# Kernel optimization log

Measured on AMD Instinct MI355X. Metric: run time of the kernel, lower is better.

## Reference

```python
import jax, jax.numpy as jnp
import numpy as np

B, S, D, F, E, R = 16, 1024, 1024, 4096, 8, 32
LORA_ALPHA = 16
SCALING = LORA_ALPHA / R  # 0.5


def setup_inputs() -> dict:
    key = jax.random.key(0)
    ks = jax.random.split(key, 16)
    sd = 0.02
    return {
        "x": jax.random.normal(ks[0], (B, S, D), jnp.float32),
        "router_w": jax.random.normal(ks[1], (E, D), jnp.float32) * sd,
        "router_b": jnp.zeros((E,), jnp.float32),
        "fc1_w": jax.random.normal(ks[2], (F, D), jnp.float32) * sd,
        "fc1_b": jnp.zeros((F,), jnp.float32),
        "fc2_w": jax.random.normal(ks[3], (D, F), jnp.float32) * sd,
        "fc2_b": jnp.zeros((D,), jnp.float32),
        "down_A_w": jax.random.normal(ks[4], (E, R, D), jnp.float32) * sd,
        "down_A_b": jnp.zeros((E, R), jnp.float32),
        "down_B_w": jax.random.normal(ks[5], (E, F, R), jnp.float32) * sd,
        "down_B_b": jnp.zeros((E, F), jnp.float32),
        "up_A_w": jax.random.normal(ks[6], (E, R, F), jnp.float32) * sd,
        "up_A_b": jnp.zeros((E, R), jnp.float32),
        "up_B_w": jax.random.normal(ks[7], (E, D, R), jnp.float32) * sd,
        "up_B_b": jnp.zeros((E, D), jnp.float32),
    }


def _lora_moe_sparse(inp, onehot, A_w, A_b, B_w, B_b):
    # inp: [b,t,c_in]; onehot: [b,t,E] hard top-1 dispatch mask
    # h: per-expert rank activations [b,t,E,R] (small: R=32)
    h = jnp.einsum('btc,erc->bter', inp, A_w) + A_b
    g = h * onehot[..., None]  # zero out non-selected experts (sparse dispatch)
    out = jnp.einsum('bter,eor->bto', g, B_w)
    out = out + jnp.einsum('bte,eo->bto', onehot, B_b)
    return out * SCALING


def reference(x, router_w, router_b, fc1_w, fc1_b, fc2_w, fc2_b,
              down_A_w, down_A_b, down_B_w, down_B_b,
              up_A_w, up_A_b, up_B_w, up_B_b):
    # router + top-1 hard routing (straight-through expert_choice)
    logits = jnp.einsum('btd,ed->bte', x, router_w) + router_b
    routing = jax.nn.softmax(logits, axis=-1)
    idx = jnp.argmax(routing, axis=-1)                       # [b,t]
    y_hard = jax.nn.one_hot(idx, E, dtype=x.dtype)           # [b,t,E]
    expert_choice = y_hard - jax.lax.stop_gradient(routing) + routing

    # down proj: frozen fc1 + sparse LoRA combine (dropout p=0.05 -> eval/identity)
    h1 = jnp.einsum('btd,fd->btf', x, fc1_w) + fc1_b
    h1 = h1 + _lora_moe_sparse(x, y_hard, down_A_w, down_A_b, down_B_w, down_B_b)
    a = jax.nn.gelu(h1, approximate=False)

    # up proj: frozen fc2 + sparse LoRA combine
    out = jnp.einsum('btf,df->btd', a, fc2_w) + fc2_b
    out = out + _lora_moe_sparse(a, y_hard, up_A_w, up_A_b, up_B_w, up_B_b)
    return out, (routing, expert_choice)
```

## Files before the change

### kernel.cpp

```cpp
#include <hip/hip_runtime.h>
#include <hip/hip_bf16.h>
#include <math.h>


#define M_TOK 16384
#define DIM_D 1024
#define DIM_F 4096
#define NEXP 8
#define RANK 32
#define NER 256

typedef __attribute__((ext_vector_type(8))) short bf16x8;
typedef __attribute__((ext_vector_type(4))) float f32x4;

__device__ inline short f2bs(float x) {
  __hip_bfloat16 h = __float2bfloat16(x);
  return *reinterpret_cast<short*>(&h);
}

__device__ inline void async16(const void* g, void* l) {
  __builtin_amdgcn_global_load_lds(
      (__attribute__((address_space(1))) void*)(g),
      (__attribute__((address_space(3))) void*)(l), 16, 0, 0);
}

__global__ __launch_bounds__(256) void convert_bf16(
    const float* __restrict__ in, short* __restrict__ out, int n8)
{
  const int i = blockIdx.x * 256 + threadIdx.x;
  if (i >= n8) return;
  const float4* p = (const float4*)in + 2 * (size_t)i;
  float4 u = p[0], v = p[1];
  bf16x8 r;
  r[0] = f2bs(u.x); r[1] = f2bs(u.y); r[2] = f2bs(u.z); r[3] = f2bs(u.w);
  r[4] = f2bs(v.x); r[5] = f2bs(v.y); r[6] = f2bs(v.z); r[7] = f2bs(v.w);
  *(bf16x8*)(out + 8 * (size_t)i) = r;
}

__global__ __launch_bounds__(256) void router_kernel(
    const float* __restrict__ X,
    const float* __restrict__ RW,
    const float* __restrict__ RB,
    float* __restrict__ routing_out,
    float* __restrict__ ec_out,
    int* __restrict__ idx_out)
{
  const int wave = threadIdx.x >> 6;
  const int lane = threadIdx.x & 63;
  const int t = blockIdx.x * 4 + wave;

  const float4* xp = (const float4*)(X + (size_t)t * DIM_D);
  float4 xv[4];
#pragma unroll
  for (int i = 0; i < 4; ++i) xv[i] = xp[lane + 64 * i];

  float logit[NEXP];
#pragma unroll
  for (int e = 0; e < NEXP; ++e) {
    const float4* wp = (const float4*)(RW + (size_t)e * DIM_D);
    double p = 0.0;
#pragma unroll
    for (int i = 0; i < 4; ++i) {
      float4 w = wp[lane + 64 * i];
      p += (double)xv[i].x * w.x + (double)xv[i].y * w.y +
           (double)xv[i].z * w.z + (double)xv[i].w * w.w;
    }
#pragma unroll
    for (int off = 32; off > 0; off >>= 1) p += __shfl_xor(p, off);
    logit[e] = (float)p + RB[e];
  }
  float m = logit[0];
  int am = 0;
#pragma unroll
  for (int e = 1; e < NEXP; ++e)
    if (logit[e] > m) { m = logit[e]; am = e; }
  float pr[NEXP], s = 0.f;
#pragma unroll
  for (int e = 0; e < NEXP; ++e) { pr[e] = expf(logit[e] - m); s += pr[e]; }
  const float inv = 1.f / s;
  if (lane < NEXP) {
    float r = pr[lane] * inv;
    routing_out[(size_t)t * NEXP + lane] = r;
    float y = (lane == am) ? 1.f : 0.f;
    ec_out[(size_t)t * NEXP + lane] = (y - r) + r;
  }
  if (lane == 0) idx_out[t] = am;
}

template <int KMAIN, int DO_LORA, int EPI>
__global__ __launch_bounds__(256, 2) void gemm_bf16(
    const short* __restrict__ A, const short* __restrict__ Bm,
    const short* __restrict__ G2, const short* __restrict__ LW,
    const float* __restrict__ LB, const float* __restrict__ bias,
    const int* __restrict__ idx, void* __restrict__ outv, int N)
{
  __shared__ __align__(16) short As[128 * 32];
  __shared__ __align__(16) short Bs[128 * 32];

  const int tid = threadIdx.x;
  const int m0 = blockIdx.y * 128;
  const int n0 = blockIdx.x * 128;
  const int lane = tid & 63;
  const int wv = tid >> 6;
  const int quad = lane >> 4;
  const int lrow = lane & 15;
  const int wr = wv >> 1;
  const int wc = wv & 1;
  const int r0 = tid >> 2;
  const int c4 = (tid & 3) * 8;

  f32x4 acc[4][4];
#pragma unroll
  for (int i = 0; i < 4; ++i)
#pragma unroll
    for (int j = 0; j < 4; ++j) acc[i][j] = (f32x4){0.f, 0.f, 0.f, 0.f};

  constexpr int IT_MAIN = KMAIN / 32;
  constexpr int IT_TOT = IT_MAIN + (DO_LORA ? NEXP : 0);
  for (int it = 0; it < IT_TOT; ++it) {
    const short *a0, *a1, *b0, *b1;
    if (!DO_LORA || it < IT_MAIN) {
      const int k = it * 32;
      a0 = A + (size_t)(m0 + r0) * KMAIN + k + c4;
      a1 = a0 + (size_t)64 * KMAIN;
      b0 = Bm + (size_t)(n0 + r0) * KMAIN + k + c4;
      b1 = b0 + (size_t)64 * KMAIN;
    } else {
      const int e = it - IT_MAIN;
      a0 = G2 + (size_t)(m0 + r0) * NER + e * RANK + c4;
      a1 = a0 + 64 * NER;
      b0 = LW + ((size_t)e * N + n0 + r0) * RANK + c4;
      b1 = b0 + 64 * RANK;
    }
    async16(a0, &As[tid * 8]);
    async16(a1, &As[2048 + tid * 8]);
    async16(b0, &Bs[tid * 8]);
    async16(b1, &Bs[2048 + tid * 8]);
    __syncthreads();

    bf16x8 af[4], bfv[4];
#pragma unroll
    for (int i = 0; i < 4; ++i)
      af[i] = *(const bf16x8*)&As[(wr * 64 + i * 16 + lrow) * 32 + quad * 8];
#pragma unroll
    for (int j = 0; j < 4; ++j)
      bfv[j] = *(const bf16x8*)&Bs[(wc * 64 + j * 16 + lrow) * 32 + quad * 8];
#pragma unroll
    for (int i = 0; i < 4; ++i)
#pragma unroll
      for (int j = 0; j < 4; ++j)
        acc[i][j] = __builtin_amdgcn_mfma_f32_16x16x32_bf16(af[i], bfv[j],
                                                            acc[i][j], 0, 0, 0);
    __syncthreads();
  }

  float cb[4];
#pragma unroll
  for (int j = 0; j < 4; ++j) cb[j] = bias[n0 + wc * 64 + j * 16 + lrow];

#pragma unroll
  for (int i = 0; i < 4; ++i) {
#pragma unroll
    for (int reg = 0; reg < 4; ++reg) {
      const int t = m0 + wr * 64 + i * 16 + quad * 4 + reg;
      const int e = idx[t];
#pragma unroll
      for (int j = 0; j < 4; ++j) {
        const int gc = n0 + wc * 64 + j * 16 + lrow;
        float v = acc[i][j][reg];
        if (EPI == 2) {
          v = ((gc >> 5) == e) ? 0.5f * (v + cb[j]) : 0.f;
          ((short*)outv)[(size_t)t * N + gc] = f2bs(v);
        } else {
          v += cb[j] + 0.5f * LB[(size_t)e * N + gc];
          if (EPI == 1) {
            v = 0.5f * v * (1.0f + erff(v * 0.70710678118654752f));
            ((short*)outv)[(size_t)t * N + gc] = f2bs(v);
          } else {
            ((float*)outv)[(size_t)t * N + gc] = v;
          }
        }
      }
    }
  }
}

extern "C" void kernel_launch(void* const* d_in, const int* in_sizes, int n_in,
                              void* d_out, int out_size, void* d_ws, size_t ws_size,
                              hipStream_t stream) {
  (void)in_sizes; (void)n_in; (void)out_size; (void)ws_size;
  const float* x        = (const float*)d_in[0];
  const float* router_w = (const float*)d_in[1];
  const float* router_b = (const float*)d_in[2];
  const float* fc1_w    = (const float*)d_in[3];
  const float* fc1_b    = (const float*)d_in[4];
  const float* fc2_w    = (const float*)d_in[5];
  const float* fc2_b    = (const float*)d_in[6];
  const float* down_A_w = (const float*)d_in[7];
  const float* down_A_b = (const float*)d_in[8];
  const float* down_B_w = (const float*)d_in[9];
  const float* down_B_b = (const float*)d_in[10];
  const float* up_A_w   = (const float*)d_in[11];
  const float* up_A_b   = (const float*)d_in[12];
  const float* up_B_w   = (const float*)d_in[13];
  const float* up_B_b   = (const float*)d_in[14];

  char* ws = (char*)d_ws;
  size_t off = 0;
  int* idxp = (int*)ws;                    off += (size_t)M_TOK * 4;
  short* g2d  = (short*)(ws + off);        off += (size_t)M_TOK * NER * 2;
  short* g2u  = (short*)(ws + off);        off += (size_t)M_TOK * NER * 2;
  short* a_ws = (short*)(ws + off);        off += (size_t)M_TOK * DIM_F * 2;
  short* xb   = (short*)(ws + off);        off += (size_t)M_TOK * DIM_D * 2;
  short* fc1b = (short*)(ws + off);        off += (size_t)DIM_F * DIM_D * 2;
  short* fc2b = (short*)(ws + off);        off += (size_t)DIM_D * DIM_F * 2;
  short* dAb  = (short*)(ws + off);        off += (size_t)NER * DIM_D * 2;
  short* uAb  = (short*)(ws + off);        off += (size_t)NER * DIM_F * 2;
  short* dBb  = (short*)(ws + off);        off += (size_t)NEXP * DIM_F * RANK * 2;
  short* uBb  = (short*)(ws + off);        off += (size_t)NEXP * DIM_D * RANK * 2;

  float* out = (float*)d_out;
  float* routing = out + (size_t)M_TOK * DIM_D;
  float* ec = routing + (size_t)M_TOK * NEXP;

  auto conv = [&](const float* src, short* dst, size_t n) {
    int n8 = (int)(n / 8);
    convert_bf16<<<(n8 + 255) / 256, 256, 0, stream>>>(src, dst, n8);
  };
  conv(x, xb, (size_t)M_TOK * DIM_D);
  conv(fc1_w, fc1b, (size_t)DIM_F * DIM_D);
  conv(fc2_w, fc2b, (size_t)DIM_D * DIM_F);
  conv(down_A_w, dAb, (size_t)NER * DIM_D);
  conv(up_A_w, uAb, (size_t)NER * DIM_F);
  conv(down_B_w, dBb, (size_t)NEXP * DIM_F * RANK);
  conv(up_B_w, uBb, (size_t)NEXP * DIM_D * RANK);

  router_kernel<<<M_TOK / 4, 256, 0, stream>>>(x, router_w, router_b, routing,
                                               ec, idxp);
  gemm_bf16<DIM_D, 0, 2><<<dim3(NER / 128, M_TOK / 128), 256, 0, stream>>>(
      xb, dAb, nullptr, nullptr, nullptr, down_A_b, idxp, g2d, NER);
  gemm_bf16<DIM_D, 1, 1><<<dim3(DIM_F / 128, M_TOK / 128), 256, 0, stream>>>(
      xb, fc1b, g2d, dBb, down_B_b, fc1_b, idxp, a_ws, DIM_F);
  gemm_bf16<DIM_F, 0, 2><<<dim3(NER / 128, M_TOK / 128), 256, 0, stream>>>(
      a_ws, uAb, nullptr, nullptr, nullptr, up_A_b, idxp, g2u, NER);
  gemm_bf16<DIM_F, 1, 0><<<dim3(DIM_D / 128, M_TOK / 128), 256, 0, stream>>>(
      a_ws, fc2b, g2u, uBb, up_B_b, fc2_b, idxp, out, DIM_D);
}
```

Measured before the change: 763.7 us.

## Concatenate LoRA into K dimension and use 256x256 pipelined GEMM

The LoRA rank activations and LoRA-B weights are packed as extra K columns of the activation and weight matrices, so the main GEMMs run a single uniform K loop. The main GEMMs move to a 512-thread, 256x256-tile kernel with double-buffered LDS, swizzled addressing, interleaved async loads and MFMA priority hints, plus workgroup remapping for L2 locality. The x-to-bf16 conversion is folded into the router kernel, removing a separate pass. The larger tile raises register and LDS pressure, and the hand-written barrier and waitcnt schedule must be exactly right.

```diff
diff --git a/kernel.cpp b/kernel.cpp
--- a/kernel.cpp
+++ b/kernel.cpp
@@ -9,8 +9,11 @@
 #define NEXP 8
 #define RANK 32
 #define NER 256
+#define K1 1280
+#define K2 4352
 
 typedef __attribute__((ext_vector_type(8))) short bf16x8;
+typedef __attribute__((ext_vector_type(4))) short sh4;
 typedef __attribute__((ext_vector_type(4))) float f32x4;
 
 __device__ inline short f2bs(float x) {
@@ -24,17 +27,38 @@
       (__attribute__((address_space(3))) void*)(l), 16, 0, 0);
 }
 
-__global__ __launch_bounds__(256) void convert_bf16(
-    const float* __restrict__ in, short* __restrict__ out, int n8)
+__global__ __launch_bounds__(256) void convert_pitched(
+    const float* __restrict__ in, short* __restrict__ out,
+    int c8, int opitch, int n8)
 {
   const int i = blockIdx.x * 256 + threadIdx.x;
   if (i >= n8) return;
-  const float4* p = (const float4*)in + 2 * (size_t)i;
+  const int row = i / c8;
+  const int c = (i % c8) * 8;
+  const float4* p = (const float4*)(in + (size_t)row * (c8 * 8) + c);
   float4 u = p[0], v = p[1];
   bf16x8 r;
   r[0] = f2bs(u.x); r[1] = f2bs(u.y); r[2] = f2bs(u.z); r[3] = f2bs(u.w);
   r[4] = f2bs(v.x); r[5] = f2bs(v.y); r[6] = f2bs(v.z); r[7] = f2bs(v.w);
-  *(bf16x8*)(out + 8 * (size_t)i) = r;
+  *(bf16x8*)(out + (size_t)row * opitch + c) = r;
+}
+
+__global__ __launch_bounds__(256) void pack_lorab(
+    const float* __restrict__ in, short* __restrict__ out,
+    int Nn, int opitch, int ooff, int n8)
+{
+  const int i = blockIdx.x * 256 + threadIdx.x;
+  if (i >= n8) return;
+  const int e = i / (Nn * 4);
+  const int rem = i % (Nn * 4);
+  const int n = rem >> 2;
+  const int r8 = (rem & 3) * 8;
+  const float4* p = (const float4*)(in + ((size_t)e * Nn + n) * RANK + r8);
+  float4 u = p[0], v = p[1];
+  bf16x8 r;
+  r[0] = f2bs(u.x); r[1] = f2bs(u.y); r[2] = f2bs(u.z); r[3] = f2bs(u.w);
+  r[4] = f2bs(v.x); r[5] = f2bs(v.y); r[6] = f2bs(v.z); r[7] = f2bs(v.w);
+  *(bf16x8*)(out + (size_t)n * opitch + ooff + e * RANK + r8) = r;
 }
 
 __global__ __launch_bounds__(256) void router_kernel(
@@ -43,7 +67,8 @@
     const float* __restrict__ RB,
     float* __restrict__ routing_out,
     float* __restrict__ ec_out,
-    int* __restrict__ idx_out)
+    int* __restrict__ idx_out,
+    short* __restrict__ XB)
 {
   const int wave = threadIdx.x >> 6;
   const int lane = threadIdx.x & 63;
@@ -53,6 +78,14 @@
   float4 xv[4];
 #pragma unroll
   for (int i = 0; i < 4; ++i) xv[i] = xp[lane + 64 * i];
+
+#pragma unroll
+  for (int i = 0; i < 4; ++i) {
+    sh4 o;
+    o[0] = f2bs(xv[i].x); o[1] = f2bs(xv[i].y);
+    o[2] = f2bs(xv[i].z); o[3] = f2bs(xv[i].w);
+    *(sh4*)&XB[(size_t)t * K1 + (lane + 64 * i) * 4] = o;
+  }
 
   float logit[NEXP];
 #pragma unroll
@@ -87,12 +120,11 @@
   if (lane == 0) idx_out[t] = am;
 }
 
-template <int KMAIN, int DO_LORA, int EPI>
-__global__ __launch_bounds__(256, 2) void gemm_bf16(
+template <int KM, int LDA, int OPITCH, int OOFF>
+__global__ __launch_bounds__(256, 2) void lora_a_gemm(
     const short* __restrict__ A, const short* __restrict__ Bm,
-    const short* __restrict__ G2, const short* __restrict__ LW,
-    const float* __restrict__ LB, const float* __restrict__ bias,
-    const int* __restrict__ idx, void* __restrict__ outv, int N)
+    const float* __restrict__ bias, const int* __restrict__ idx,
+    short* __restrict__ out)
 {
   __shared__ __align__(16) short As[128 * 32];
   __shared__ __align__(16) short Bs[128 * 32];
@@ -115,27 +147,14 @@
 #pragma unroll
     for (int j = 0; j < 4; ++j) acc[i][j] = (f32x4){0.f, 0.f, 0.f, 0.f};
 
-  constexpr int IT_MAIN = KMAIN / 32;
-  constexpr int IT_TOT = IT_MAIN + (DO_LORA ? NEXP : 0);
-  for (int it = 0; it < IT_TOT; ++it) {
-    const short *a0, *a1, *b0, *b1;
-    if (!DO_LORA || it < IT_MAIN) {
-      const int k = it * 32;
-      a0 = A + (size_t)(m0 + r0) * KMAIN + k + c4;
-      a1 = a0 + (size_t)64 * KMAIN;
-      b0 = Bm + (size_t)(n0 + r0) * KMAIN + k + c4;
-      b1 = b0 + (size_t)64 * KMAIN;
-    } else {
-      const int e = it - IT_MAIN;
-      a0 = G2 + (size_t)(m0 + r0) * NER + e * RANK + c4;
-      a1 = a0 + 64 * NER;
-      b0 = LW + ((size_t)e * N + n0 + r0) * RANK + c4;
-      b1 = b0 + 64 * RANK;
-    }
+  for (int it = 0; it < KM / 32; ++it) {
+    const int k = it * 32;
+    const short* a0 = A + (size_t)(m0 + r0) * LDA + k + c4;
+    const short* b0 = Bm + (size_t)(n0 + r0) * KM + k + c4;
     async16(a0, &As[tid * 8]);
-    async16(a1, &As[2048 + tid * 8]);
+    async16(a0 + (size_t)64 * LDA, &As[2048 + tid * 8]);
     async16(b0, &Bs[tid * 8]);
-    async16(b1, &Bs[2048 + tid * 8]);
+    async16(b0 + (size_t)64 * KM, &Bs[2048 + tid * 8]);
     __syncthreads();
 
     bf16x8 af[4], bfv[4];
@@ -167,18 +186,140 @@
 #pragma unroll
       for (int j = 0; j < 4; ++j) {
         const int gc = n0 + wc * 64 + j * 16 + lrow;
-        float v = acc[i][j][reg];
-        if (EPI == 2) {
-          v = ((gc >> 5) == e) ? 0.5f * (v + cb[j]) : 0.f;
-          ((short*)outv)[(size_t)t * N + gc] = f2bs(v);
+        float v = ((gc >> 5) == e) ? 0.5f * (acc[i][j][reg] + cb[j]) : 0.f;
+        out[(size_t)t * OPITCH + OOFF + gc] = f2bs(v);
+      }
+    }
+  }
+}
+
+template <int K, int N, int POUT, int EPI>
+__global__ __launch_bounds__(512, 2) void gemm256(
+    const short* __restrict__ A, const short* __restrict__ Bm,
+    const float* __restrict__ LB, const float* __restrict__ bias,
+    const int* __restrict__ idx, void* __restrict__ outv)
+{
+  static_assert(K % 128 == 0, "K must be multiple of 128");
+  __shared__ __align__(16) short lds[65536];
+
+  const int tid = threadIdx.x;
+  const int lane = tid & 63;
+  const int wv = tid >> 6;
+  const int wr = wv >> 2;
+  const int wc = wv & 3;
+  const int quad = lane >> 4;
+  const int lrow = lane & 15;
+
+  const int gx = gridDim.x;
+  int id = blockIdx.y * gx + blockIdx.x;
+  const int nwg = gx * gridDim.y;
+  id = (id & 7) * (nwg >> 3) + (id >> 3);
+  const int m0 = (id / gx) * 256;
+  const int n0 = (id % gx) * 256;
+
+  const int srow = wv * 32 + (lane >> 2);
+  const int scol = ((lane & 3) * 8) ^ ((lane >= 32) ? 16 : 0);
+  const short* Asrc = A + (size_t)(m0 + srow) * K + scol;
+  const short* Bsrc = Bm + (size_t)(n0 + srow) * K + scol;
+  const int sdst = wv * 1024 + lane * 8;
+
+  const int innerA = (lrow * 32 + quad * 8) ^ ((lrow & 8) ? 16 : 0);
+  const int aoff = wr * 4096 + innerA;
+  const int boff = 16384 + wc * 2048 + innerA;
+
+  f32x4 acc[8][4];
+#pragma unroll
+  for (int i = 0; i < 8; ++i)
+#pragma unroll
+    for (int j = 0; j < 4; ++j) acc[i][j] = (f32x4){0.f, 0.f, 0.f, 0.f};
+
+  bf16x8 af[4], bfv[4];
+
+#define STG(src, t, h, tens, buf)                                              \
+  {                                                                            \
+    _Pragma("unroll") for (int jj = 0; jj < 2; ++jj)                           \
+        async16((src) + (size_t)(jj * 16) * K + (t) * 64 + (h) * 32,           \
+                &lds[(buf) * 32768 + (tens) + (h) * 8192 + sdst + jj * 512]);  \
+  }
+#define RDB(ks, buf)                                                           \
+  _Pragma("unroll") for (int j = 0; j < 4; ++j)                                \
+      bfv[j] = *(const bf16x8*)&lds[(buf) * 32768 + (ks) * 8192 + boff + j * 512];
+#define RDA(mh, ks, buf)                                                       \
+  _Pragma("unroll") for (int i = 0; i < 4; ++i)                                \
+      af[i] = *(const bf16x8*)&lds[(buf) * 32768 + (ks) * 8192 + aoff +        \
+                                   ((mh) * 4 + i) * 512];
+#define MM(mh)                                                                 \
+  {                                                                            \
+    __builtin_amdgcn_s_setprio(1);                                             \
+    _Pragma("unroll") for (int i = 0; i < 4; ++i)                              \
+    _Pragma("unroll") for (int j = 0; j < 4; ++j)                              \
+        acc[(mh) * 4 + i][j] = __builtin_amdgcn_mfma_f32_16x16x32_bf16(        \
+            af[i], bfv[j], acc[(mh) * 4 + i][j], 0, 0, 0);                     \
+    __builtin_amdgcn_s_setprio(0);                                             \
+  }
+#define BARR asm volatile("s_barrier" ::: "memory")
+#define WV4 asm volatile("s_waitcnt vmcnt(4)" ::: "memory")
+#define WV0 asm volatile("s_waitcnt vmcnt(0)" ::: "memory")
+
+  STG(Asrc, 0, 0, 0, 0);
+  STG(Bsrc, 0, 0, 16384, 0);
+  STG(Asrc, 0, 1, 0, 0);
+  STG(Bsrc, 0, 1, 16384, 0);
+  WV4; BARR;
+
+  constexpr int nIter = K / 128;
+  for (int it = 0; it < nIter - 1; ++it) {
+    const int t1 = 2 * it + 1, t2 = 2 * it + 2;
+    RDB(0, 0); RDA(0, 0, 0); STG(Asrc, t1, 0, 0, 1);     BARR; MM(0);      BARR;
+    RDA(1, 0, 0);            STG(Bsrc, t1, 0, 16384, 1); BARR; MM(1); WV4; BARR;
+    RDB(1, 0); RDA(0, 1, 0); STG(Asrc, t1, 1, 0, 1);     BARR; MM(0);      BARR;
+    RDA(1, 1, 0);            STG(Bsrc, t1, 1, 16384, 1); BARR; MM(1); WV4; BARR;
+    RDB(0, 1); RDA(0, 0, 1); STG(Asrc, t2, 0, 0, 0);     BARR; MM(0);      BARR;
+    RDA(1, 0, 1);            STG(Bsrc, t2, 0, 16384, 0); BARR; MM(1); WV4; BARR;
+    RDB(1, 1); RDA(0, 1, 1); STG(Asrc, t2, 1, 0, 0);     BARR; MM(0);      BARR;
+    RDA(1, 1, 1);            STG(Bsrc, t2, 1, 16384, 0); BARR; MM(1); WV4; BARR;
+  }
+  {
+    const int t1 = 2 * nIter - 1;
+    RDB(0, 0); RDA(0, 0, 0); STG(Asrc, t1, 0, 0, 1);     BARR; MM(0);      BARR;
+    RDA(1, 0, 0);            STG(Bsrc, t1, 0, 16384, 1); BARR; MM(1); WV4; BARR;
+    RDB(1, 0); RDA(0, 1, 0); STG(Asrc, t1, 1, 0, 1);     BARR; MM(0);      BARR;
+    RDA(1, 1, 0);            STG(Bsrc, t1, 1, 16384, 1); BARR; MM(1); WV4; BARR;
+    RDB(0, 1); RDA(0, 0, 1);                             BARR; MM(0);      BARR;
+    RDA(1, 0, 1);                                        BARR; MM(1); WV0; BARR;
+    RDB(1, 1); RDA(0, 1, 1);                             BARR; MM(0);      BARR;
+    RDA(1, 1, 1);                                        BARR; MM(1);
+  }
+#undef STG
+#undef RDB
+#undef RDA
+#undef MM
+#undef BARR
+#undef WV4
+#undef WV0
+
+  const int orow0 = m0 + wr * 128;
+  const int ocol0 = n0 + wc * 64;
+  float cb[4];
+#pragma unroll
+  for (int j = 0; j < 4; ++j) cb[j] = bias[ocol0 + j * 16 + lrow];
+
+#pragma unroll
+  for (int i = 0; i < 8; ++i) {
+#pragma unroll
+    for (int reg = 0; reg < 4; ++reg) {
+      const int t = orow0 + i * 16 + quad * 4 + reg;
+      const int e = idx[t];
+      const float* lbp = LB + (size_t)e * N;
+#pragma unroll
+      for (int j = 0; j < 4; ++j) {
+        const int gc = ocol0 + j * 16 + lrow;
+        float v = acc[i][j][reg] + cb[j] + 0.5f * lbp[gc];
+        if (EPI == 1) {
+          v = 0.5f * v * (1.0f + erff(v * 0.70710678118654752f));
+          ((short*)outv)[(size_t)t * POUT + gc] = f2bs(v);
         } else {
-          v += cb[j] + 0.5f * LB[(size_t)e * N + gc];
-          if (EPI == 1) {
-            v = 0.5f * v * (1.0f + erff(v * 0.70710678118654752f));
-            ((short*)outv)[(size_t)t * N + gc] = f2bs(v);
-          } else {
-            ((float*)outv)[(size_t)t * N + gc] = v;
-          }
+          ((float*)outv)[(size_t)t * POUT + gc] = v;
         }
       }
     }
@@ -207,42 +348,35 @@
 
   char* ws = (char*)d_ws;
   size_t off = 0;
-  int* idxp = (int*)ws;                    off += (size_t)M_TOK * 4;
-  short* g2d  = (short*)(ws + off);        off += (size_t)M_TOK * NER * 2;
-  short* g2u  = (short*)(ws + off);        off += (size_t)M_TOK * NER * 2;
-  short* a_ws = (short*)(ws + off);        off += (size_t)M_TOK * DIM_F * 2;
-  short* xb   = (short*)(ws + off);        off += (size_t)M_TOK * DIM_D * 2;
-  short* fc1b = (short*)(ws + off);        off += (size_t)DIM_F * DIM_D * 2;
-  short* fc2b = (short*)(ws + off);        off += (size_t)DIM_D * DIM_F * 2;
-  short* dAb  = (short*)(ws + off);        off += (size_t)NER * DIM_D * 2;
-  short* uAb  = (short*)(ws + off);        off += (size_t)NER * DIM_F * 2;
-  short* dBb  = (short*)(ws + off);        off += (size_t)NEXP * DIM_F * RANK * 2;
-  short* uBb  = (short*)(ws + off);        off += (size_t)NEXP * DIM_D * RANK * 2;
+  int* idxp  = (int*)ws;              off += (size_t)M_TOK * 4;
+  short* xbw = (short*)(ws + off);    off += (size_t)M_TOK * K1 * 2;
+  short* aw  = (short*)(ws + off);    off += (size_t)M_TOK * K2 * 2;
+  short* B1w = (short*)(ws + off);    off += (size_t)DIM_F * K1 * 2;
+  short* B2w = (short*)(ws + off);    off += (size_t)DIM_D * K2 * 2;
+  short* dAb = (short*)(ws + off);    off += (size_t)NER * DIM_D * 2;
+  short* uAb = (short*)(ws + off);    off += (size_t)NER * DIM_F * 2;
 
   float* out = (float*)d_out;
   float* routing = out + (size_t)M_TOK * DIM_D;
   float* ec = routing + (size_t)M_TOK * NEXP;
 
-  auto conv = [&](const float* src, short* dst, size_t n) {
-    int n8 = (int)(n / 8);
-    convert_bf16<<<(n8 + 255) / 256, 256, 0, stream>>>(src, dst, n8);
-  };
-  conv(x, xb, (size_t)M_TOK * DIM_D);
-  conv(fc1_w, fc1b, (size_t)DIM_F * DIM_D);
-  conv(fc2_w, fc2b, (size_t)DIM_D * DIM_F);
-  conv(down_A_w, dAb, (size_t)NER * DIM_D);
-  conv(up_A_w, uAb, (size_t)NER * DIM_F);
-  conv(down_B_w, dBb, (size_t)NEXP * DIM_F * RANK);
-  conv(up_B_w, uBb, (size_t)NEXP * DIM_D * RANK);
+  convert_pitched<<<2048, 256, 0, stream>>>(fc1_w, B1w, 128, K1, 524288);
+  convert_pitched<<<2048, 256, 0, stream>>>(fc2_w, B2w, 512, K2, 524288);
+  convert_pitched<<<128,  256, 0, stream>>>(down_A_w, dAb, 128, DIM_D, 32768);
+  convert_pitched<<<512,  256, 0, stream>>>(up_A_w,   uAb, 512, DIM_F, 131072);
+  pack_lorab<<<512, 256, 0, stream>>>(down_B_w, B1w, DIM_F, K1, DIM_D, 131072);
+  pack_lorab<<<128, 256, 0, stream>>>(up_B_w,   B2w, DIM_D, K2, DIM_F, 32768);
 
   router_kernel<<<M_TOK / 4, 256, 0, stream>>>(x, router_w, router_b, routing,
-                                               ec, idxp);
-  gemm_bf16<DIM_D, 0, 2><<<dim3(NER / 128, M_TOK / 128), 256, 0, stream>>>(
-      xb, dAb, nullptr, nullptr, nullptr, down_A_b, idxp, g2d, NER);
-  gemm_bf16<DIM_D, 1, 1><<<dim3(DIM_F / 128, M_TOK / 128), 256, 0, stream>>>(
-      xb, fc1b, g2d, dBb, down_B_b, fc1_b, idxp, a_ws, DIM_F);
-  gemm_bf16<DIM_F, 0, 2><<<dim3(NER / 128, M_TOK / 128), 256, 0, stream>>>(
-      a_ws, uAb, nullptr, nullptr, nullptr, up_A_b, idxp, g2u, NER);
-  gemm_bf16<DIM_F, 1, 0><<<dim3(DIM_D / 128, M_TOK / 128), 256, 0, stream>>>(
-      a_ws, fc2b, g2u, uBb, up_B_b, fc2_b, idxp, out, DIM_D);
-}
+                                               ec, idxp, xbw);
+  lora_a_gemm<DIM_D, K1, K1, DIM_D>
+      <<<dim3(2, M_TOK / 128), 256, 0, stream>>>(xbw, dAb, down_A_b, idxp, xbw);
+  gemm256<K1, DIM_F, K2, 1>
+      <<<dim3(DIM_F / 256, M_TOK / 256), 512, 0, stream>>>(
+          xbw, B1w, down_B_b, fc1_b, idxp, aw);
+  lora_a_gemm<DIM_F, K2, K2, DIM_F>
+      <<<dim3(2, M_TOK / 128), 256, 0, stream>>>(aw, uAb, up_A_b, idxp, aw);
+  gemm256<K2, DIM_D, DIM_D, 0>
+      <<<dim3(DIM_D / 256, M_TOK / 256), 512, 0, stream>>>(
+          aw, B2w, up_B_b, fc2_b, idxp, out);
+}
```

Result: faster. 678.5 us (-11.2%).
